# Kernel tuning notes

Measured on AMD Instinct MI355X. Metric: run time of the kernel, lower is better.

## Reference

```python
import jax, jax.numpy as jnp
import numpy as np

RBF_CO = 10.077141124806595


def setup_inputs() -> dict:
    key = jax.random.key(0)
    k1, k2, k3 = jax.random.split(key, 3)
    n, dim = 2048, 128
    N, out_dim = 50000, 64
    features = jax.random.normal(k1, (n, dim), dtype=jnp.float32)
    train_data = jax.random.normal(k2, (N, dim), dtype=jnp.float32)
    weights = jax.random.normal(k3, (N, out_dim), dtype=jnp.float32) * 0.02
    return {"features": features, "train_data": train_data, "weights": weights}


def reference(features, train_data, weights):
    x2 = jnp.sum(features * features, axis=-1, keepdims=True)      # [n, 1]
    t2 = jnp.sum(train_data * train_data, axis=-1)                 # [N]
    d2 = x2 + t2[None, :] - 2.0 * (features @ train_data.T)        # [n, N]
    dist = jnp.sqrt(jnp.maximum(d2, 0.0))                          # clamp fp error
    k = jnp.exp(-dist / RBF_CO / 2.0)                              # RBF kernel [n, N]
    return k @ weights                                              # [n, out_dim]
```

## Files before the change

### kernel.cpp

```cpp
#include <hip/hip_runtime.h>
#include <hip/hip_bf16.h>
#include <stdint.h>

#define DIM 128
#define ODIM 64
#define BM 128
#define BN 64

typedef __attribute__((ext_vector_type(8))) __bf16 bf16x8;
typedef __attribute__((ext_vector_type(4))) __bf16 bf16x4;
typedef __attribute__((ext_vector_type(2))) __bf16 bf16x2;
typedef __attribute__((ext_vector_type(4))) float f32x4;

#define MFMA_K32(a, b, c) __builtin_amdgcn_mfma_f32_16x16x32_bf16((a), (b), (c), 0, 0, 0)
#define MFMA_K16(a, b, c) __builtin_amdgcn_mfma_f32_16x16x16bf16_1k((a), (b), (c), 0, 0, 0)

#define RBFD 10.077141124806595
#define LOG2E 1.4426950408889634
#define C2D ((LOG2E / (2.0 * RBFD)) * (LOG2E / (2.0 * RBFD)))

__device__ __forceinline__ void async_copy16(const void* g, void* l) {
  __builtin_amdgcn_global_load_lds((const __attribute__((address_space(1))) void*)g,
                                   (__attribute__((address_space(3))) void*)l, 16, 0, 0);
}
__device__ __forceinline__ void async_copy4(const void* g, void* l) {
  __builtin_amdgcn_global_load_lds((const __attribute__((address_space(1))) void*)g,
                                   (__attribute__((address_space(3))) void*)l, 4, 0, 0);
}

__device__ __forceinline__ uint32_t pack_bf16(float a, float b) {
  uint32_t ua = __builtin_bit_cast(uint32_t, a) + 0x8000u;
  uint32_t ub = __builtin_bit_cast(uint32_t, b) + 0x8000u;
  return __builtin_amdgcn_perm(ub, ua, 0x07060302u);
}

__global__ void prep_all(const float* __restrict__ train, __bf16* __restrict__ Tb,
                         float* __restrict__ t2, const float* __restrict__ feat,
                         __bf16* __restrict__ Fb, float* __restrict__ x2,
                         const float* __restrict__ W, __bf16* __restrict__ Wt,
                         int Ntrain, int Npad, int nFeat, int tB, int fB, float scale) {
  __shared__ float tile[64][65];
  int b = blockIdx.x;
  int t = threadIdx.x;
  if (b < tB + fB) {
    const float* src;
    __bf16* dst;
    float* sq;
    int nValid, nPad, row0;
    float padv;
    if (b < tB) {
      src = train; dst = Tb; sq = t2; nValid = Ntrain; nPad = Npad; row0 = b * 4; padv = 1e30f;
    } else {
      src = feat; dst = Fb; sq = x2; nValid = nFeat; nPad = nFeat; row0 = (b - tB) * 4; padv = 0.0f;
    }
    int row = row0 + (t >> 6);
    int lane = t & 63;
    if (row >= nPad) return;
    float2 v = make_float2(0.0f, 0.0f);
    if (row < nValid) v = ((const float2*)src)[(size_t)row * 64 + lane];
    bf16x2 p;
    p.x = (__bf16)v.x;
    p.y = (__bf16)v.y;
    *(bf16x2*)&dst[(size_t)row * DIM + lane * 2] = p;
    float ss = v.x * v.x + v.y * v.y;
    #pragma unroll
    for (int off = 32; off > 0; off >>= 1) ss += __shfl_down(ss, off);
    if (lane == 0) sq[row] = (row < nValid) ? ss * scale : padv;
    return;
  }
  int j0 = (b - tB - fB) * 64;
  int jr = t >> 2;
  int cg = (t & 3) * 16;
  int j = j0 + jr;
  if (j < Ntrain) {
    const float4* src = (const float4*)(W + (size_t)j * ODIM);
    #pragma unroll
    for (int q = 0; q < 4; ++q) {
      float4 u = src[(cg >> 2) + q];
      tile[jr][cg + q * 4 + 0] = u.x;
      tile[jr][cg + q * 4 + 1] = u.y;
      tile[jr][cg + q * 4 + 2] = u.z;
      tile[jr][cg + q * 4 + 3] = u.w;
    }
  } else {
    #pragma unroll
    for (int q = 0; q < 16; ++q) tile[jr][cg + q] = 0.0f;
  }
  __syncthreads();
  int v = t >> 2;
  int jc = (t & 3) * 16;
  __bf16 ob[16];
  #pragma unroll
  for (int q = 0; q < 16; ++q) ob[q] = (__bf16)tile[jc + q][v];
  __bf16* dst = Wt + (size_t)v * Npad + j0 + jc;
  *(bf16x8*)dst = *(bf16x8*)&ob[0];
  *(bf16x8*)(dst + 8) = *(bf16x8*)&ob[8];
}

template <int NS, bool ATOMIC>
__global__ __launch_bounds__(256, 4) void rbf_main(
    const __bf16* __restrict__ Fb, const __bf16* __restrict__ Tb,
    const __bf16* __restrict__ Wt, const float* __restrict__ t2g,
    const float* __restrict__ x2g, float* __restrict__ outOrPart,
    int nRows, int Npad, int nChunks) {
  __shared__ __bf16 sT[BN * DIM];
  __shared__ __bf16 sW[ODIM * BN];
  __shared__ float st2[BN];

  const int tid = threadIdx.x;
  const int wave = tid >> 6;
  const int lane = tid & 63;
  const int l16 = lane & 15;
  const int g4 = lane >> 4;

  const int ns = (int)blockIdx.x;
  const int mb = (int)blockIdx.y;

  constexpr float KNEG2 = (float)(-2.0 * C2D);

  int aOff[4];
  #pragma unroll
  for (int ko = 0; ko < 4; ++ko) aOff[ko] = l16 * 256 + (((ko * 4 + g4) ^ l16) << 4);
  int wOff[4];
  #pragma unroll
  for (int mt = 0; mt < 4; ++mt)
    wOff[mt] = l16 * 128 + ((g4 & 1) << 3) + ((((2 * mt + (g4 >> 1)) ^ (l16 & 7))) << 4);

  int tGOff[4], ldsOffT[4];
  #pragma unroll
  for (int i = 0; i < 4; ++i) {
    int off = i * 4096 + wave * 1024;
    int loff = off + lane * 16;
    int row = loff >> 8;
    int gran = (loff >> 4) & 15;
    ldsOffT[i] = off;
    tGOff[i] = row * 256 + ((gran ^ (row & 15)) << 4);
  }
  int wGOff[2], ldsOffW[2];
  #pragma unroll
  for (int i = 0; i < 2; ++i) {
    int off = i * 4096 + wave * 1024;
    int loff = off + lane * 16;
    int v = loff >> 7;
    int gran = (loff >> 4) & 7;
    ldsOffW[i] = off;
    wGOff[i] = v * (Npad * 2) + ((gran ^ (v & 7)) << 4);
  }
  const char* gTbase = (const char*)Tb + (size_t)ns * (BN * 256);
  const char* gWbase = (const char*)Wt + (size_t)ns * (BN * 2);
  const char* gt2 = (const char*)(t2g) + (size_t)ns * (BN * 4) + lane * 4;
  const size_t strT = (size_t)NS * (BN * 256);
  const size_t strW = (size_t)NS * (BN * 2);
  const size_t str2 = (size_t)NS * (BN * 4);

  bf16x8 bF[2][4];
  #pragma unroll
  for (int nf = 0; nf < 2; ++nf)
    #pragma unroll
    for (int ko = 0; ko < 4; ++ko)
      bF[nf][ko] = *(const bf16x8*)(Fb + ((size_t)(mb * BM + wave * 32 + nf * 16 + l16)) * DIM +
                                    ko * 32 + g4 * 8);
  float x2v[2];
  #pragma unroll
  for (int nf = 0; nf < 2; ++nf)
    x2v[nf] = x2g[mb * BM + wave * 32 + nf * 16 + l16];

  f32x4 zero4 = {0.0f, 0.0f, 0.0f, 0.0f};
  f32x4 oacc[2][4];
  #pragma unroll
  for (int nf = 0; nf < 2; ++nf)
    #pragma unroll
    for (int vi = 0; vi < 4; ++vi) oacc[nf][vi] = zero4;

  for (int c = ns; c < nChunks; c += NS) {
    #pragma unroll
    for (int i = 0; i < 4; ++i) async_copy16(gTbase + tGOff[i], (char*)sT + ldsOffT[i]);
    #pragma unroll
    for (int i = 0; i < 2; ++i) async_copy16(gWbase + wGOff[i], (char*)sW + ldsOffW[i]);
    if (wave == 0) async_copy4(gt2, (char*)st2);
    gTbase += strT;
    gWbase += strW;
    gt2 += str2;
    __syncthreads();

    uint2 pk[4][2];
    #pragma unroll
    for (int mt = 0; mt < 4; ++mt) {
      f32x4 s0 = zero4, s1 = zero4;
      #pragma unroll
      for (int ko = 0; ko < 4; ++ko) {
        bf16x8 a = *(const bf16x8*)((const char*)sT + aOff[ko] + mt * 4096);
        s0 = MFMA_K32(a, bF[0][ko], s0);
        s1 = MFMA_K32(a, bF[1][ko], s1);
      }
      f32x4 t2v = *(const f32x4*)&st2[mt * 16 + g4 * 4];
      float kv0[4], kv1[4];
      #pragma unroll
      for (int r = 0; r < 4; ++r) {
        float d20 = __builtin_fmaf(KNEG2, s0[r], t2v[r] + x2v[0]);
        float d21 = __builtin_fmaf(KNEG2, s1[r], t2v[r] + x2v[1]);
        kv0[r] = __builtin_amdgcn_exp2f(-__builtin_amdgcn_sqrtf(d20));
        kv1[r] = __builtin_amdgcn_exp2f(-__builtin_amdgcn_sqrtf(d21));
      }
      pk[mt][0] = make_uint2(pack_bf16(kv0[0], kv0[1]), pack_bf16(kv0[2], kv0[3]));
      pk[mt][1] = make_uint2(pack_bf16(kv1[0], kv1[1]), pack_bf16(kv1[2], kv1[3]));
    }

    #pragma unroll
    for (int vi = 0; vi < 4; ++vi) {
      #pragma unroll
      for (int mt = 0; mt < 4; ++mt) {
        bf16x4 wf = *(const bf16x4*)((const char*)sW + wOff[mt] + vi * 2048);
        oacc[0][vi] = MFMA_K16(__builtin_bit_cast(bf16x4, pk[mt][0]), wf, oacc[0][vi]);
        oacc[1][vi] = MFMA_K16(__builtin_bit_cast(bf16x4, pk[mt][1]), wf, oacc[1][vi]);
      }
    }
    __syncthreads();
  }

  if (ATOMIC) {
    float* out = outOrPart;
    #pragma unroll
    for (int nf = 0; nf < 2; ++nf)
      #pragma unroll
      for (int vi = 0; vi < 4; ++vi)
        #pragma unroll
        for (int r = 0; r < 4; ++r) {
          int row = mb * BM + wave * 32 + nf * 16 + g4 * 4 + r;
          int col = vi * 16 + l16;
          atomicAdd(&out[(size_t)row * ODIM + col], oacc[nf][vi][r]);
        }
  } else {
    float* dst = outOrPart + (size_t)ns * (size_t)nRows * ODIM;
    #pragma unroll
    for (int nf = 0; nf < 2; ++nf)
      #pragma unroll
      for (int vi = 0; vi < 4; ++vi)
        #pragma unroll
        for (int r = 0; r < 4; ++r) {
          int row = mb * BM + wave * 32 + nf * 16 + g4 * 4 + r;
          int col = vi * 16 + l16;
          dst[(size_t)row * ODIM + col] = oacc[nf][vi][r];
        }
  }
}

template <int NS>
__global__ void reduce_parts(const float4* __restrict__ part, float4* __restrict__ out,
                             int total4) {
  int i = (int)blockIdx.x * blockDim.x + threadIdx.x;
  if (i >= total4) return;
  float4 s = make_float4(0.0f, 0.0f, 0.0f, 0.0f);
  #pragma unroll
  for (int sp = 0; sp < NS; ++sp) {
    float4 v = part[(size_t)sp * total4 + i];
    s.x += v.x; s.y += v.y; s.z += v.z; s.w += v.w;
  }
  out[i] = s;
}

extern "C" void kernel_launch(void* const* d_in, const int* in_sizes, int n_in,
                              void* d_out, int out_size, void* d_ws, size_t ws_size,
                              hipStream_t stream) {
  (void)n_in;
  const float* features = (const float*)d_in[0];
  const float* train = (const float*)d_in[1];
  const float* weights = (const float*)d_in[2];
  float* out = (float*)d_out;

  const int n = in_sizes[0] / DIM;
  const int N = in_sizes[1] / DIM;
  const int Npad = ((N + 63) / 64) * 64;
  const int nChunks = Npad / 64;

  size_t off = 0;
  auto alloc = [&](size_t bytes) {
    size_t o = off;
    off = (off + bytes + 255) & ~(size_t)255;
    return o;
  };
  size_t oT = alloc((size_t)Npad * DIM * 2);
  size_t oW = alloc((size_t)ODIM * Npad * 2);
  size_t oF = alloc((size_t)n * DIM * 2);
  size_t ot2 = alloc((size_t)Npad * 4);
  size_t ox2 = alloc((size_t)n * 4);
  size_t bufEnd = off;
  size_t oPart = alloc(0);

  char* ws = (char*)d_ws;
  __bf16* Tb = (__bf16*)(ws + oT);
  __bf16* Wt = (__bf16*)(ws + oW);
  __bf16* Fb = (__bf16*)(ws + oF);
  float* t2 = (float*)(ws + ot2);
  float* x2 = (float*)(ws + ox2);
  float* part = (float*)(ws + oPart);

  const int tB = Npad / 4;
  const int fB = n / 4;
  const int wB = Npad / 64;
  prep_all<<<tB + fB + wB, 256, 0, stream>>>(train, Tb, t2, features, Fb, x2, weights, Wt,
                                             N, Npad, n, tB, fB, (float)C2D);

  const int mBlocks = n / BM;
  const int total4 = n * ODIM / 4;
  const size_t partBytes = (size_t)n * ODIM * 4;

  if (ws_size >= bufEnd + 96 * partBytes) {
    rbf_main<96, false><<<dim3(96, mBlocks), 256, 0, stream>>>(Fb, Tb, Wt, t2, x2, part, n,
                                                               Npad, nChunks);
    reduce_parts<96><<<(total4 + 255) / 256, 256, 0, stream>>>((const float4*)part,
                                                               (float4*)out, total4);
  } else if (ws_size >= bufEnd + 32 * partBytes) {
    rbf_main<32, false><<<dim3(32, mBlocks), 256, 0, stream>>>(Fb, Tb, Wt, t2, x2, part, n,
                                                               Npad, nChunks);
    reduce_parts<32><<<(total4 + 255) / 256, 256, 0, stream>>>((const float4*)part,
                                                               (float4*)out, total4);
  } else {
    hipMemsetAsync(d_out, 0, (size_t)out_size * sizeof(float), stream);
    rbf_main<96, true><<<dim3(96, mBlocks), 256, 0, stream>>>(Fb, Tb, Wt, t2, x2, out, n,
                                                              Npad, nChunks);
  }
}
```

Baseline: 148.5 us.

## Double-buffer LDS tiles, fuse split reduction via last-block counter, halve N-splits

The main loop now uses two LDS buffers, so the async loads for the next train/weight chunk are issued before computing the current one. This overlaps global-to-LDS transfer with MFMA and exp work. The separate reduce_parts kernel is removed: each block bumps a per-row-block atomic counter, and the last arriving block sums all partial slabs into the output. The split count drops from 96 to 48, which halves partial traffic but gives fewer blocks and doubles LDS use per block, possibly hurting occupancy.

After: 276.0 us. +85.8%, slower.

```diff
diff --git a/kernel.cpp b/kernel.cpp
--- a/kernel.cpp
+++ b/kernel.cpp
@@ -38,10 +38,12 @@
                          float* __restrict__ t2, const float* __restrict__ feat,
                          __bf16* __restrict__ Fb, float* __restrict__ x2,
                          const float* __restrict__ W, __bf16* __restrict__ Wt,
+                         uint32_t* __restrict__ cnt,
                          int Ntrain, int Npad, int nFeat, int tB, int fB, float scale) {
   __shared__ float tile[64][65];
   int b = blockIdx.x;
   int t = threadIdx.x;
+  if (b == 0 && t < 16) cnt[t] = 0;
   if (b < tB + fB) {
     const float* src;
     __bf16* dst;
@@ -101,11 +103,13 @@
 __global__ __launch_bounds__(256, 4) void rbf_main(
     const __bf16* __restrict__ Fb, const __bf16* __restrict__ Tb,
     const __bf16* __restrict__ Wt, const float* __restrict__ t2g,
-    const float* __restrict__ x2g, float* __restrict__ outOrPart,
+    const float* __restrict__ x2g, float* __restrict__ part,
+    float* __restrict__ outF, uint32_t* __restrict__ cnt,
     int nRows, int Npad, int nChunks) {
-  __shared__ __bf16 sT[BN * DIM];
-  __shared__ __bf16 sW[ODIM * BN];
-  __shared__ float st2[BN];
+  __shared__ __bf16 sT[2][BN * DIM];
+  __shared__ __bf16 sW[2][ODIM * BN];
+  __shared__ float st2[2][BN];
+  __shared__ int lastFlag;
 
   const int tid = threadIdx.x;
   const int wave = tid >> 6;
@@ -172,28 +176,44 @@
     #pragma unroll
     for (int vi = 0; vi < 4; ++vi) oacc[nf][vi] = zero4;
 
+  #pragma unroll
+  for (int i = 0; i < 4; ++i) async_copy16(gTbase + tGOff[i], (char*)sT[0] + ldsOffT[i]);
+  #pragma unroll
+  for (int i = 0; i < 2; ++i) async_copy16(gWbase + wGOff[i], (char*)sW[0] + ldsOffW[i]);
+  if (wave == 0) async_copy4(gt2, (char*)st2[0]);
+  gTbase += strT;
+  gWbase += strW;
+  gt2 += str2;
+  __syncthreads();
+
+  int buf = 0;
   for (int c = ns; c < nChunks; c += NS) {
-    #pragma unroll
-    for (int i = 0; i < 4; ++i) async_copy16(gTbase + tGOff[i], (char*)sT + ldsOffT[i]);
-    #pragma unroll
-    for (int i = 0; i < 2; ++i) async_copy16(gWbase + wGOff[i], (char*)sW + ldsOffW[i]);
-    if (wave == 0) async_copy4(gt2, (char*)st2);
-    gTbase += strT;
-    gWbase += strW;
-    gt2 += str2;
-    __syncthreads();
-
+    if (c + NS < nChunks) {
+      #pragma unroll
+      for (int i = 0; i < 4; ++i)
+        async_copy16(gTbase + tGOff[i], (char*)sT[buf ^ 1] + ldsOffT[i]);
+      #pragma unroll
+      for (int i = 0; i < 2; ++i)
+        async_copy16(gWbase + wGOff[i], (char*)sW[buf ^ 1] + ldsOffW[i]);
+      if (wave == 0) async_copy4(gt2, (char*)st2[buf ^ 1]);
+      gTbase += strT;
+      gWbase += strW;
+      gt2 += str2;
+    }
+
+    const char* sTb = (const char*)sT[buf];
+    const char* sWb = (const char*)sW[buf];
     uint2 pk[4][2];
     #pragma unroll
     for (int mt = 0; mt < 4; ++mt) {
       f32x4 s0 = zero4, s1 = zero4;
       #pragma unroll
       for (int ko = 0; ko < 4; ++ko) {
-        bf16x8 a = *(const bf16x8*)((const char*)sT + aOff[ko] + mt * 4096);
+        bf16x8 a = *(const bf16x8*)(sTb + aOff[ko] + mt * 4096);
         s0 = MFMA_K32(a, bF[0][ko], s0);
         s1 = MFMA_K32(a, bF[1][ko], s1);
       }
-      f32x4 t2v = *(const f32x4*)&st2[mt * 16 + g4 * 4];
+      f32x4 t2v = *(const f32x4*)&st2[buf][mt * 16 + g4 * 4];
       float kv0[4], kv1[4];
       #pragma unroll
       for (int r = 0; r < 4; ++r) {
@@ -210,16 +230,17 @@
     for (int vi = 0; vi < 4; ++vi) {
       #pragma unroll
       for (int mt = 0; mt < 4; ++mt) {
-        bf16x4 wf = *(const bf16x4*)((const char*)sW + wOff[mt] + vi * 2048);
+        bf16x4 wf = *(const bf16x4*)(sWb + wOff[mt] + vi * 2048);
         oacc[0][vi] = MFMA_K16(__builtin_bit_cast(bf16x4, pk[mt][0]), wf, oacc[0][vi]);
         oacc[1][vi] = MFMA_K16(__builtin_bit_cast(bf16x4, pk[mt][1]), wf, oacc[1][vi]);
       }
     }
+
     __syncthreads();
+    buf ^= 1;
   }
 
   if (ATOMIC) {
-    float* out = outOrPart;
     #pragma unroll
     for (int nf = 0; nf < 2; ++nf)
       #pragma unroll
@@ -228,10 +249,10 @@
         for (int r = 0; r < 4; ++r) {
           int row = mb * BM + wave * 32 + nf * 16 + g4 * 4 + r;
           int col = vi * 16 + l16;
-          atomicAdd(&out[(size_t)row * ODIM + col], oacc[nf][vi][r]);
+          atomicAdd(&outF[(size_t)row * ODIM + col], oacc[nf][vi][r]);
         }
   } else {
-    float* dst = outOrPart + (size_t)ns * (size_t)nRows * ODIM;
+    float* dst = part + (size_t)ns * (size_t)nRows * ODIM;
     #pragma unroll
     for (int nf = 0; nf < 2; ++nf)
       #pragma unroll
@@ -242,21 +263,26 @@
           int col = vi * 16 + l16;
           dst[(size_t)row * ODIM + col] = oacc[nf][vi][r];
         }
-  }
-}
-
-template <int NS>
-__global__ void reduce_parts(const float4* __restrict__ part, float4* __restrict__ out,
-                             int total4) {
-  int i = (int)blockIdx.x * blockDim.x + threadIdx.x;
-  if (i >= total4) return;
-  float4 s = make_float4(0.0f, 0.0f, 0.0f, 0.0f);
-  #pragma unroll
-  for (int sp = 0; sp < NS; ++sp) {
-    float4 v = part[(size_t)sp * total4 + i];
-    s.x += v.x; s.y += v.y; s.z += v.z; s.w += v.w;
-  }
-  out[i] = s;
+    __threadfence();
+    if (tid == 0) lastFlag = (atomicAdd(&cnt[mb], 1u) == (uint32_t)(NS - 1)) ? 1 : 0;
+    __syncthreads();
+    if (lastFlag) {
+      __threadfence();
+      const int slab4 = nRows * ODIM / 4;
+      const int base4 = mb * BM * ODIM / 4;
+      const float4* p4 = (const float4*)part;
+      float4* o4 = (float4*)outF;
+      for (int i = tid; i < BM * ODIM / 4; i += 256) {
+        float4 s = make_float4(0.0f, 0.0f, 0.0f, 0.0f);
+        #pragma unroll 4
+        for (int sp = 0; sp < NS; ++sp) {
+          float4 v = p4[(size_t)sp * slab4 + base4 + i];
+          s.x += v.x; s.y += v.y; s.z += v.z; s.w += v.w;
+        }
+        o4[base4 + i] = s;
+      }
+    }
+  }
 }
 
 extern "C" void kernel_launch(void* const* d_in, const int* in_sizes, int n_in,
@@ -284,6 +310,7 @@
   size_t oF = alloc((size_t)n * DIM * 2);
   size_t ot2 = alloc((size_t)Npad * 4);
   size_t ox2 = alloc((size_t)n * 4);
+  size_t oCnt = alloc(64);
   size_t bufEnd = off;
   size_t oPart = alloc(0);
 
@@ -293,31 +320,27 @@
   __bf16* Fb = (__bf16*)(ws + oF);
   float* t2 = (float*)(ws + ot2);
   float* x2 = (float*)(ws + ox2);
+  uint32_t* cnt = (uint32_t*)(ws + oCnt);
   float* part = (float*)(ws + oPart);
 
   const int tB = Npad / 4;
   const int fB = n / 4;
   const int wB = Npad / 64;
   prep_all<<<tB + fB + wB, 256, 0, stream>>>(train, Tb, t2, features, Fb, x2, weights, Wt,
-                                             N, Npad, n, tB, fB, (float)C2D);
+                                             cnt, N, Npad, n, tB, fB, (float)C2D);
 
   const int mBlocks = n / BM;
-  const int total4 = n * ODIM / 4;
   const size_t partBytes = (size_t)n * ODIM * 4;
 
-  if (ws_size >= bufEnd + 96 * partBytes) {
-    rbf_main<96, false><<<dim3(96, mBlocks), 256, 0, stream>>>(Fb, Tb, Wt, t2, x2, part, n,
-                                                               Npad, nChunks);
-    reduce_parts<96><<<(total4 + 255) / 256, 256, 0, stream>>>((const float4*)part,
-                                                               (float4*)out, total4);
+  if (ws_size >= bufEnd + 48 * partBytes) {
+    rbf_main<48, false><<<dim3(48, mBlocks), 256, 0, stream>>>(Fb, Tb, Wt, t2, x2, part, out,
+                                                               cnt, n, Npad, nChunks);
   } else if (ws_size >= bufEnd + 32 * partBytes) {
-    rbf_main<32, false><<<dim3(32, mBlocks), 256, 0, stream>>>(Fb, Tb, Wt, t2, x2, part, n,
-                                                               Npad, nChunks);
-    reduce_parts<32><<<(total4 + 255) / 256, 256, 0, stream>>>((const float4*)part,
-                                                               (float4*)out, total4);
+    rbf_main<32, false><<<dim3(32, mBlocks), 256, 0, stream>>>(Fb, Tb, Wt, t2, x2, part, out,
+                                                               cnt, n, Npad, nChunks);
   } else {
     hipMemsetAsync(d_out, 0, (size_t)out_size * sizeof(float), stream);
-    rbf_main<96, true><<<dim3(96, mBlocks), 256, 0, stream>>>(Fb, Tb, Wt, t2, x2, out, n,
-                                                              Npad, nChunks);
-  }
-}
+    rbf_main<48, true><<<dim3(48, mBlocks), 256, 0, stream>>>(Fb, Tb, Wt, t2, x2, part, out,
+                                                              cnt, n, Npad, nChunks);
+  }
+}
```
